# Kernel tuning notes

Hardware: AMD Instinct MI355X
Metric: run time of the kernel (lower is better)

The kernel has to match this reference:

```python
import jax, jax.numpy as jnp
import numpy as np

D_MODEL = 1024
NHEAD = 16
HEAD_DIM = D_MODEL // NHEAD
D_FF = 4096
EPS = 1e-5


def _layernorm(x, g, b):
    mu = jnp.mean(x, axis=-1, keepdims=True)
    var = jnp.mean((x - mu) ** 2, axis=-1, keepdims=True)
    return (x - mu) * jax.lax.rsqrt(var + EPS) * g + b


def setup_inputs() -> dict:
    key = jax.random.key(0)
    ks = jax.random.split(key, 13)
    s = 1.0 / np.sqrt(D_MODEL)
    sf = 1.0 / np.sqrt(D_FF)
    # weights stored as [in, out] (transposed torch Linear)
    return {
        "src": jax.random.normal(ks[0], (4, 2048, D_MODEL), jnp.float32),
        "Wq": jax.random.uniform(ks[1], (D_MODEL, D_MODEL), jnp.float32, -s, s),
        "bq": jnp.zeros((D_MODEL,), jnp.float32),
        "Wk": jax.random.uniform(ks[2], (D_MODEL, D_MODEL), jnp.float32, -s, s),
        "bk": jnp.zeros((D_MODEL,), jnp.float32),
        "Wv": jax.random.uniform(ks[3], (D_MODEL, D_MODEL), jnp.float32, -s, s),
        "bv": jnp.zeros((D_MODEL,), jnp.float32),
        "Wo": jax.random.uniform(ks[4], (D_MODEL, D_MODEL), jnp.float32, -s, s),
        "bo": jnp.zeros((D_MODEL,), jnp.float32),
        "W1": jax.random.uniform(ks[5], (D_MODEL, D_FF), jnp.float32, -s, s),
        "b1": jnp.zeros((D_FF,), jnp.float32),
        "W2": jax.random.uniform(ks[6], (D_FF, D_MODEL), jnp.float32, -sf, sf),
        "b2": jnp.zeros((D_MODEL,), jnp.float32),
        "g1": jnp.ones((D_MODEL,), jnp.float32),
        "be1": jnp.zeros((D_MODEL,), jnp.float32),
        "g2": jnp.ones((D_MODEL,), jnp.float32),
        "be2": jnp.zeros((D_MODEL,), jnp.float32),
    }


def reference(src, Wq, bq, Wk, bk, Wv, bv, Wo, bo, W1, b1, W2, b2, g1, be1, g2, be2):
    B, S, _ = src.shape
    scale = 1.0 / np.sqrt(HEAD_DIM)
    # project and split heads: [B, H, S, Dh]
    def heads(W, b):
        return (src @ W + b).reshape(B, S, NHEAD, HEAD_DIM).transpose(0, 2, 1, 3)
    Q, K, V = heads(Wq, bq), heads(Wk, bk), heads(Wv, bv)
    scores = jnp.einsum('bhqd,bhkd->bhqk', Q, K) * scale
    attn = jax.nn.softmax(scores, axis=-1)
    ctx = jnp.einsum('bhqk,bhkd->bhqd', attn, V)
    ctx = ctx.transpose(0, 2, 1, 3).reshape(B, S, D_MODEL)
    attn_out = ctx @ Wo + bo
    x = _layernorm(src + attn_out, g1, be1)
    ff = jax.nn.relu(x @ W1 + b1) @ W2 + b2
    return _layernorm(x + ff, g2, be2)
```

## Files before the change

### kernel.cpp

```cpp
#include <hip/hip_runtime.h>

typedef __attribute__((ext_vector_type(8))) short bf16x8;
typedef __attribute__((ext_vector_type(4))) float f32x4;
typedef unsigned short u16;
typedef unsigned int u32;

__device__ __forceinline__ u16 f2b(float f) {
  u32 u = __float_as_uint(f);
  u = (u + 0x7fffu + ((u >> 16) & 1u)) >> 16;
  return (u16)u;
}
__device__ __forceinline__ float b2f(u16 b) {
  return __uint_as_float(((u32)b) << 16);
}
__device__ __forceinline__ u32 cvtpk_bf16(float lo, float hi) {
  u32 r;
  asm("v_cvt_pk_bf16_f32 %0, %1, %2" : "=v"(r) : "v"(lo), "v"(hi));
  return r;
}
__device__ __forceinline__ void gload_lds16(const u16* g, u16* l) {
  __builtin_amdgcn_global_load_lds(
      (const __attribute__((address_space(1))) void*)g,
      (__attribute__((address_space(3))) void*)l, 16, 0, 0);
}

__global__ __launch_bounds__(256) void cvt_bf16(const float* __restrict__ in,
                                                u16* __restrict__ out, int n4) {
  int i = blockIdx.x * 256 + threadIdx.x;
  if (i >= n4) return;
  float4 v = ((const float4*)in)[i];
  ushort4 o;
  o.x = f2b(v.x); o.y = f2b(v.y); o.z = f2b(v.z); o.w = f2b(v.w);
  ((ushort4*)out)[i] = o;
}

__global__ __launch_bounds__(256) void transpose_w(const float* __restrict__ in,
                                                   u16* __restrict__ out,
                                                   int R, int C) {
  __shared__ float t[32][33];
  int tid = threadIdx.x, tx = tid & 31, ty = tid >> 5;
  int rb = blockIdx.y * 32, cb = blockIdx.x * 32;
  for (int i = 0; i < 4; i++)
    t[ty + i * 8][tx] = in[(size_t)(rb + ty + i * 8) * C + cb + tx];
  __syncthreads();
  for (int i = 0; i < 4; i++)
    out[(size_t)(cb + ty + i * 8) * R + rb + tx] = f2b(t[tx][ty + i * 8]);
}

__global__ __launch_bounds__(256) void concat3(const float* __restrict__ a,
                                               const float* __restrict__ b,
                                               const float* __restrict__ c,
                                               float* __restrict__ o) {
  int i = blockIdx.x * 256 + threadIdx.x;
  if (i >= 3072) return;
  o[i] = i < 1024 ? a[i] : (i < 2048 ? b[i - 1024] : c[i - 2048]);
}

__device__ __forceinline__ void stage_quarter(const u16* __restrict__ src,
                                              size_t rowbase, int K, int kcol,
                                              u16* dst, int c, int srow, int sg,
                                              int wid) {
  int row_ = c * 64 + srow;
  int gs_ = sg ^ (row_ & 7);
  gload_lds16(src + (rowbase + row_) * K + kcol + gs_ * 8,
              &dst[(c * 64 + wid * 8) * 64]);
}

template <bool PF>
__device__ __forceinline__ void tile_step(
    const u16* sAc, const u16* sBc, u16* sAn, u16* sBn,
    const u16* __restrict__ A, const u16* __restrict__ Bt, size_t abase,
    size_t bbase, int K, int Tn, int wm, int wn, int l16, int lq, int srow,
    int sg, int wid, f32x4 (&acc)[8][4]) {
  __syncthreads();
#pragma unroll
  for (int ks = 0; ks < 2; ++ks) {
    bf16x8 Bf[4], Af[4];
#pragma unroll
    for (int j = 0; j < 4; ++j) {
      int r = wn * 64 + j * 16 + l16;
      Bf[j] = *(const bf16x8*)&sBc[r * 64 + (((ks * 4 + lq) ^ (r & 7)) << 3)];
    }
#pragma unroll
    for (int i = 0; i < 4; ++i) {
      int r = wm * 128 + i * 16 + l16;
      Af[i] = *(const bf16x8*)&sAc[r * 64 + (((ks * 4 + lq) ^ (r & 7)) << 3)];
    }
    if (PF) {
      const u16* src = (ks == 0) ? A : Bt;
      size_t rb = (ks == 0) ? abase : bbase;
      u16* dst = (ks == 0) ? sAn : sBn;
      stage_quarter(src, rb, K, Tn * 64, dst, 0, srow, sg, wid);
      stage_quarter(src, rb, K, Tn * 64, dst, 1, srow, sg, wid);
    }
    __builtin_amdgcn_s_setprio(1);
#pragma unroll
    for (int i = 0; i < 4; ++i)
#pragma unroll
      for (int j = 0; j < 4; ++j)
        acc[i][j] = __builtin_amdgcn_mfma_f32_16x16x32_bf16(Af[i], Bf[j],
                                                            acc[i][j], 0, 0, 0);
    __builtin_amdgcn_s_setprio(0);
#pragma unroll
    for (int i = 0; i < 4; ++i) {
      int r = wm * 128 + 64 + i * 16 + l16;
      Af[i] = *(const bf16x8*)&sAc[r * 64 + (((ks * 4 + lq) ^ (r & 7)) << 3)];
    }
    if (PF) {
      const u16* src = (ks == 0) ? A : Bt;
      size_t rb = (ks == 0) ? abase : bbase;
      u16* dst = (ks == 0) ? sAn : sBn;
      stage_quarter(src, rb, K, Tn * 64, dst, 2, srow, sg, wid);
      stage_quarter(src, rb, K, Tn * 64, dst, 3, srow, sg, wid);
    }
    __builtin_amdgcn_s_setprio(1);
#pragma unroll
    for (int i = 0; i < 4; ++i)
#pragma unroll
      for (int j = 0; j < 4; ++j)
        acc[4 + i][j] = __builtin_amdgcn_mfma_f32_16x16x32_bf16(
            Af[i], Bf[j], acc[4 + i][j], 0, 0, 0);
    __builtin_amdgcn_s_setprio(0);
  }
}

template <int MODE>
__global__ __launch_bounds__(512, 1) void gemm256(const u16* __restrict__ A,
                                                  const u16* __restrict__ Bt,
                                                  const float* __restrict__ bias,
                                                  void* __restrict__ out,
                                                  int M, int N, int K,
                                                  float oscale) {
  __shared__ u16 sA0[256 * 64];
  __shared__ u16 sB0[256 * 64];
  __shared__ u16 sA1[256 * 64];
  __shared__ u16 sB1[256 * 64];
  const int tid = threadIdx.x, lane = tid & 63, wid = tid >> 6;
  const int l16 = lane & 15, lq = lane >> 4;
  const int wm = wid >> 2, wn = wid & 3;
  const size_t abase = (size_t)blockIdx.x * 256;
  const size_t bbase = (size_t)blockIdx.y * 256;
  const int srow = tid >> 3;
  const int sg = tid & 7;
  const int nt = K >> 6;

  f32x4 acc[8][4];
#pragma unroll
  for (int i = 0; i < 8; ++i)
#pragma unroll
    for (int j = 0; j < 4; ++j) acc[i][j] = (f32x4){0.f, 0.f, 0.f, 0.f};

#pragma unroll
  for (int c = 0; c < 4; ++c) {
    stage_quarter(A, abase, K, 0, sA0, c, srow, sg, wid);
    stage_quarter(Bt, bbase, K, 0, sB0, c, srow, sg, wid);
  }

  int T = 0;
  for (; T + 2 < nt; T += 2) {
    tile_step<true>(sA0, sB0, sA1, sB1, A, Bt, abase, bbase, K, T + 1, wm, wn,
                    l16, lq, srow, sg, wid, acc);
    tile_step<true>(sA1, sB1, sA0, sB0, A, Bt, abase, bbase, K, T + 2, wm, wn,
                    l16, lq, srow, sg, wid, acc);
  }
  tile_step<true>(sA0, sB0, sA1, sB1, A, Bt, abase, bbase, K, nt - 1, wm, wn,
                  l16, lq, srow, sg, wid, acc);
  tile_step<false>(sA1, sB1, sA0, sB0, A, Bt, abase, bbase, K, 0, wm, wn, l16,
                   lq, srow, sg, wid, acc);

  const int gmb = blockIdx.x * 256 + wm * 128;
  const int gnb = blockIdx.y * 256 + wn * 64;
#pragma unroll
  for (int i = 0; i < 8; ++i) {
    int gm0 = gmb + i * 16 + lq * 4;
#pragma unroll
    for (int j = 0; j < 4; ++j) {
      int gn = gnb + j * 16 + l16;
      float bv = bias[gn];
#pragma unroll
      for (int r = 0; r < 4; ++r) {
        float v = acc[i][j][r] + bv;
        ((u16*)out)[(size_t)(gm0 + r) * N + gn] = f2b(v > 0.f ? v : 0.f);
      }
    }
  }
}

template <bool PF>
__device__ __forceinline__ void tile_stepR(
    const u16* sAc, const u16* sBc, u16* sAn, u16* sBn,
    const u16* __restrict__ A, const u16* __restrict__ Bt, size_t abase,
    size_t bbase, int K, int Tn, int wm, int wn, int l16, int lq, int srow,
    int sg, int wid, f32x4 (&acc)[4][4]) {
  __syncthreads();
#pragma unroll
  for (int ks = 0; ks < 2; ++ks) {
    bf16x8 Bf[4], Af[4];
#pragma unroll
    for (int j = 0; j < 4; ++j) {
      int r = wn * 64 + j * 16 + l16;
      Bf[j] = *(const bf16x8*)&sBc[r * 64 + (((ks * 4 + lq) ^ (r & 7)) << 3)];
    }
#pragma unroll
    for (int i = 0; i < 4; ++i) {
      int r = wm * 64 + i * 16 + l16;
      Af[i] = *(const bf16x8*)&sAc[r * 64 + (((ks * 4 + lq) ^ (r & 7)) << 3)];
    }
    if (PF) {
      if (ks == 0) {
        stage_quarter(A, abase, K, Tn * 64, sAn, 0, srow, sg, wid);
        stage_quarter(A, abase, K, Tn * 64, sAn, 1, srow, sg, wid);
        stage_quarter(Bt, bbase, K, Tn * 64, sBn, 0, srow, sg, wid);
      } else {
        stage_quarter(Bt, bbase, K, Tn * 64, sBn, 1, srow, sg, wid);
        stage_quarter(Bt, bbase, K, Tn * 64, sBn, 2, srow, sg, wid);
        stage_quarter(Bt, bbase, K, Tn * 64, sBn, 3, srow, sg, wid);
      }
    }
    __builtin_amdgcn_s_setprio(1);
#pragma unroll
    for (int i = 0; i < 4; ++i)
#pragma unroll
      for (int j = 0; j < 4; ++j)
        acc[i][j] = __builtin_amdgcn_mfma_f32_16x16x32_bf16(Af[i], Bf[j],
                                                            acc[i][j], 0, 0, 0);
    __builtin_amdgcn_s_setprio(0);
  }
}

template <int MODE>
__global__ __launch_bounds__(512, 1) void gemmR(const u16* __restrict__ A,
                                                const u16* __restrict__ Bt,
                                                const float* __restrict__ bias,
                                                void* __restrict__ out,
                                                int M, int N, int K,
                                                float oscale) {
  __shared__ u16 sA0[128 * 64];
  __shared__ u16 sB0[256 * 64];
  __shared__ u16 sA1[128 * 64];
  __shared__ u16 sB1[256 * 64];
  const int tid = threadIdx.x, lane = tid & 63, wid = tid >> 6;
  const int l16 = lane & 15, lq = lane >> 4;
  const int wm = wid >> 2, wn = wid & 3;
  const size_t abase = (size_t)blockIdx.x * 128;
  const size_t bbase = (size_t)blockIdx.y * 256;
  const int srow = tid >> 3;
  const int sg = tid & 7;
  const int nt = K >> 6;

  f32x4 acc[4][4];
#pragma unroll
  for (int i = 0; i < 4; ++i)
#pragma unroll
    for (int j = 0; j < 4; ++j) acc[i][j] = (f32x4){0.f, 0.f, 0.f, 0.f};

#pragma unroll
  for (int c = 0; c < 2; ++c) stage_quarter(A, abase, K, 0, sA0, c, srow, sg, wid);
#pragma unroll
  for (int c = 0; c < 4; ++c) stage_quarter(Bt, bbase, K, 0, sB0, c, srow, sg, wid);

  int T = 0;
  for (; T + 2 < nt; T += 2) {
    tile_stepR<true>(sA0, sB0, sA1, sB1, A, Bt, abase, bbase, K, T + 1, wm, wn,
                     l16, lq, srow, sg, wid, acc);
    tile_stepR<true>(sA1, sB1, sA0, sB0, A, Bt, abase, bbase, K, T + 2, wm, wn,
                     l16, lq, srow, sg, wid, acc);
  }
  tile_stepR<true>(sA0, sB0, sA1, sB1, A, Bt, abase, bbase, K, nt - 1, wm, wn,
                   l16, lq, srow, sg, wid, acc);
  tile_stepR<false>(sA1, sB1, sA0, sB0, A, Bt, abase, bbase, K, 0, wm, wn, l16,
                    lq, srow, sg, wid, acc);

  const int gmb = blockIdx.x * 128 + wm * 64;
  const int gnb = blockIdx.y * 256 + wn * 64;
#pragma unroll
  for (int i = 0; i < 4; ++i) {
    int gm0 = gmb + i * 16 + lq * 4;
#pragma unroll
    for (int j = 0; j < 4; ++j) {
      int gn = gnb + j * 16 + l16;
      float bv = bias[gn];
      if constexpr (MODE == 1) {
#pragma unroll
        for (int r = 0; r < 4; ++r)
          ((u16*)out)[(size_t)(gm0 + r) * N + gn] = f2b(acc[i][j][r] + bv);
      } else {
        int sel = gn >> 10;
        int h = (gn & 1023) >> 6, d = gn & 63;
        int b = gm0 >> 11, s = gm0 & 2047;
        u16* o = (u16*)out + (size_t)sel * (8u << 20);
        if (sel == 2) {
          ushort4 w;
          w.x = f2b(acc[i][j][0] + bv);
          w.y = f2b(acc[i][j][1] + bv);
          w.z = f2b(acc[i][j][2] + bv);
          w.w = f2b(acc[i][j][3] + bv);
          *(ushort4*)(o + ((size_t)((b * 16 + h) * 64 + d)) * 2048 + s) = w;
        } else {
          float sc = (sel == 0) ? oscale : 1.f;
#pragma unroll
          for (int r = 0; r < 4; ++r)
            o[((size_t)(b * 16 + h) * 2048 + s + r) * 64 + d] =
                f2b((acc[i][j][r] + bv) * sc);
        }
      }
    }
  }
}

__global__ __launch_bounds__(256) void attn_fwd(const u16* __restrict__ Q,
                                                const u16* __restrict__ Kb,
                                                const u16* __restrict__ Vt,
                                                u16* __restrict__ ctx) {
  __shared__ u16 sK[64][64];
  __shared__ u16 sV[64][64];
  __shared__ u16 sP[4][16][72];
  const int tid = threadIdx.x, lane = tid & 63, wid = tid >> 6;
  const int l16 = lane & 15, lq = lane >> 4;
  const int bh = blockIdx.y, qt = blockIdx.x;
  const size_t base = (size_t)bh * (2048 * 64);
  const int xk = l16 & 7;

  bf16x8 qf[2];
  {
    int qrow = qt * 64 + wid * 16 + l16;
    qf[0] = *(const bf16x8*)(Q + base + (size_t)qrow * 64 + lq * 8);
    qf[1] = *(const bf16x8*)(Q + base + (size_t)qrow * 64 + 32 + lq * 8);
  }
  f32x4 o[4];
#pragma unroll
  for (int j = 0; j < 4; j++) o[j] = (f32x4){0.f, 0.f, 0.f, 0.f};
  float mrow = -3e38f, lrow = 0.f;

  const int srow_c = lane >> 3;
  const int sslot = ((lane & 7) ^ srow_c) * 8;

  for (int kv0 = 0; kv0 < 2048; kv0 += 64) {
    __syncthreads();
#pragma unroll
    for (int c = 0; c < 2; c++) {
      int row = wid * 16 + c * 8 + srow_c;
      gload_lds16(Kb + base + (size_t)(kv0 + row) * 64 + sslot, &sK[wid * 16 + c * 8][0]);
      gload_lds16(Vt + base + (size_t)row * 2048 + kv0 + sslot, &sV[wid * 16 + c * 8][0]);
    }
    __syncthreads();

    f32x4 sf[4];
#pragma unroll
    for (int j = 0; j < 4; j++) sf[j] = (f32x4){0.f, 0.f, 0.f, 0.f};
#pragma unroll
    for (int ks = 0; ks < 2; ks++)
#pragma unroll
      for (int j = 0; j < 4; j++) {
        bf16x8 kf = *(const bf16x8*)&sK[j * 16 + l16][((ks * 4 + lq) ^ xk) * 8];
        sf[j] = __builtin_amdgcn_mfma_f32_16x16x32_bf16(kf, qf[ks], sf[j], 0, 0, 0);
      }

    float pm = fmaxf(fmaxf(fmaxf(sf[0][0], sf[0][1]), fmaxf(sf[0][2], sf[0][3])),
                     fmaxf(fmaxf(sf[1][0], sf[1][1]), fmaxf(sf[1][2], sf[1][3])));
    pm = fmaxf(pm,
               fmaxf(fmaxf(fmaxf(sf[2][0], sf[2][1]), fmaxf(sf[2][2], sf[2][3])),
                     fmaxf(fmaxf(sf[3][0], sf[3][1]), fmaxf(sf[3][2], sf[3][3]))));
    pm = fmaxf(pm, __shfl_xor(pm, 16));
    pm = fmaxf(pm, __shfl_xor(pm, 32));

    if (!__all(pm - mrow <= 8.f)) {
      float mn = fmaxf(mrow, pm);
      float osc = __builtin_amdgcn_exp2f(mrow - mn);
      mrow = mn;
      lrow *= osc;
      float oscr[4];
#pragma unroll
      for (int r = 0; r < 4; r++) oscr[r] = __shfl(osc, lq * 4 + r);
#pragma unroll
      for (int j = 0; j < 4; j++)
#pragma unroll
        for (int r = 0; r < 4; r++) o[j][r] *= oscr[r];
    }

    float rs = 0.f;
#pragma unroll
    for (int j = 0; j < 4; j++) {
      float p0 = __builtin_amdgcn_exp2f(sf[j][0] - mrow);
      float p1 = __builtin_amdgcn_exp2f(sf[j][1] - mrow);
      float p2 = __builtin_amdgcn_exp2f(sf[j][2] - mrow);
      float p3 = __builtin_amdgcn_exp2f(sf[j][3] - mrow);
      rs += (p0 + p1) + (p2 + p3);
      uint2 w;
      w.x = cvtpk_bf16(p0, p1);
      w.y = cvtpk_bf16(p2, p3);
      *(uint2*)&sP[wid][l16][j * 16 + lq * 4] = w;
    }
    rs += __shfl_xor(rs, 16);
    rs += __shfl_xor(rs, 32);
    lrow += rs;

#pragma unroll
    for (int ks = 0; ks < 2; ks++) {
      bf16x8 pf = *(const bf16x8*)&sP[wid][l16][ks * 32 + lq * 8];
#pragma unroll
      for (int j = 0; j < 4; j++) {
        bf16x8 vf = *(const bf16x8*)&sV[j * 16 + l16][((ks * 4 + lq) ^ xk) * 8];
        o[j] = __builtin_amdgcn_mfma_f32_16x16x32_bf16(pf, vf, o[j], 0, 0, 0);
      }
    }
  }

  float lval[4];
#pragma unroll
  for (int r = 0; r < 4; r++) lval[r] = 1.f / __shfl(lrow, lq * 4 + r);
  const int b = bh >> 4, h = bh & 15;
#pragma unroll
  for (int j = 0; j < 4; j++)
#pragma unroll
    for (int r = 0; r < 4; r++) {
      int srow = qt * 64 + wid * 16 + lq * 4 + r;
      int d = j * 16 + l16;
      ctx[((size_t)(b * 2048 + srow)) * 1024 + h * 64 + d] = f2b(o[j][r] * lval[r]);
    }
}

template <int A_BF16, int B_BF16, int WRITE_F32>
__global__ __launch_bounds__(256) void ln_res(const void* __restrict__ a,
                                              const void* __restrict__ bsrc,
                                              const float* __restrict__ g,
                                              const float* __restrict__ be,
                                              float* __restrict__ outf,
                                              u16* __restrict__ outb) {
  const int row = blockIdx.x, tid = threadIdx.x;
  const size_t off = (size_t)row * 1024 + tid * 4;
  float4 x;
  if constexpr (A_BF16) {
    ushort4 av = *(const ushort4*)((const u16*)a + off);
    x.x = b2f(av.x); x.y = b2f(av.y); x.z = b2f(av.z); x.w = b2f(av.w);
  } else {
    x = *(const float4*)((const float*)a + off);
  }
  if constexpr (B_BF16) {
    ushort4 bv = *(const ushort4*)((const u16*)bsrc + off);
    x.x += b2f(bv.x); x.y += b2f(bv.y); x.z += b2f(bv.z); x.w += b2f(bv.w);
  } else {
    float4 bb = *(const float4*)((const float*)bsrc + off);
    x.x += bb.x; x.y += bb.y; x.z += bb.z; x.w += bb.w;
  }
  float s = x.x + x.y + x.z + x.w;
  float s2 = x.x * x.x + x.y * x.y + x.z * x.z + x.w * x.w;
  for (int o = 1; o < 64; o <<= 1) {
    s += __shfl_xor(s, o);
    s2 += __shfl_xor(s2, o);
  }
  __shared__ float rbuf[8];
  int lane = tid & 63, wid = tid >> 6;
  if (lane == 0) { rbuf[wid] = s; rbuf[4 + wid] = s2; }
  __syncthreads();
  s = rbuf[0] + rbuf[1] + rbuf[2] + rbuf[3];
  s2 = rbuf[4] + rbuf[5] + rbuf[6] + rbuf[7];
  float mu = s * (1.f / 1024.f);
  float var = s2 * (1.f / 1024.f) - mu * mu;
  float rstd = rsqrtf(var + 1e-5f);
  int c = tid * 4;
  float y0 = (x.x - mu) * rstd * g[c + 0] + be[c + 0];
  float y1 = (x.y - mu) * rstd * g[c + 1] + be[c + 1];
  float y2 = (x.z - mu) * rstd * g[c + 2] + be[c + 2];
  float y3 = (x.w - mu) * rstd * g[c + 3] + be[c + 3];
  if constexpr (WRITE_F32) {
    float4 y; y.x = y0; y.y = y1; y.z = y2; y.w = y3;
    *(float4*)(outf + off) = y;
  } else {
    ushort4 yb;
    yb.x = f2b(y0); yb.y = f2b(y1); yb.z = f2b(y2); yb.w = f2b(y3);
    *(ushort4*)(outb + off) = yb;
  }
}

extern "C" void kernel_launch(void* const* d_in, const int* in_sizes, int n_in,
                              void* d_out, int out_size, void* d_ws, size_t ws_size,
                              hipStream_t stream) {
  const float* src = (const float*)d_in[0];
  const float* Wq = (const float*)d_in[1];
  const float* bq = (const float*)d_in[2];
  const float* Wk = (const float*)d_in[3];
  const float* bk = (const float*)d_in[4];
  const float* Wv = (const float*)d_in[5];
  const float* bv = (const float*)d_in[6];
  const float* Wo = (const float*)d_in[7];
  const float* bo = (const float*)d_in[8];
  const float* W1 = (const float*)d_in[9];
  const float* b1 = (const float*)d_in[10];
  const float* W2 = (const float*)d_in[11];
  const float* b2 = (const float*)d_in[12];
  const float* g1 = (const float*)d_in[13];
  const float* be1 = (const float*)d_in[14];
  const float* g2 = (const float*)d_in[15];
  const float* be2 = (const float*)d_in[16];
  float* out = (float*)d_out;
  char* ws = (char*)d_ws;
  const size_t MB = 1ull << 20;

  u16* XB    = (u16*)(ws + 0);
  u16* WQKVT = (u16*)(ws + 16 * MB);
  u16* WOT   = (u16*)(ws + 22 * MB);
  u16* W1T   = (u16*)(ws + 24 * MB);
  u16* W2T   = (u16*)(ws + 32 * MB);
  float* bqkv = (float*)(ws + 40 * MB);
  u16* Qb    = (u16*)(ws + 41 * MB);
  u16* Kbuf  = (u16*)(ws + 57 * MB);
  u16* Vt    = (u16*)(ws + 73 * MB);
  u16* CTX   = XB;
  u16* AO    = (u16*)(ws + 41 * MB);
  u16* H1    = (u16*)(ws + 57 * MB);
  u16* XBUF  = (u16*)(ws + 121 * MB);
  u16* FF    = XB;

  const float QSCALE = 0.125f * 1.44269504088896340736f;

  cvt_bf16<<<dim3(8192), dim3(256), 0, stream>>>(src, XB, 2097152);
  transpose_w<<<dim3(32, 32), dim3(256), 0, stream>>>(Wq, WQKVT, 1024, 1024);
  transpose_w<<<dim3(32, 32), dim3(256), 0, stream>>>(Wk, WQKVT + 1024 * 1024, 1024, 1024);
  transpose_w<<<dim3(32, 32), dim3(256), 0, stream>>>(Wv, WQKVT + 2048 * 1024, 1024, 1024);
  transpose_w<<<dim3(32, 32), dim3(256), 0, stream>>>(Wo, WOT, 1024, 1024);
  transpose_w<<<dim3(128, 32), dim3(256), 0, stream>>>(W1, W1T, 1024, 4096);
  transpose_w<<<dim3(32, 128), dim3(256), 0, stream>>>(W2, W2T, 4096, 1024);
  concat3<<<dim3(12), dim3(256), 0, stream>>>(bq, bk, bv, bqkv);

  gemmR<6><<<dim3(64, 12), dim3(512), 0, stream>>>(XB, WQKVT, bqkv, Qb,
                                                   8192, 3072, 1024, QSCALE);
  attn_fwd<<<dim3(32, 64), dim3(256), 0, stream>>>(Qb, Kbuf, Vt, CTX);
  gemmR<1><<<dim3(64, 4), dim3(512), 0, stream>>>(CTX, WOT, bo, AO,
                                                  8192, 1024, 1024, 1.0f);
  ln_res<0, 1, 0><<<dim3(8192), dim3(256), 0, stream>>>(src, AO, g1, be1, nullptr, XBUF);
  gemm256<2><<<dim3(32, 16), dim3(512), 0, stream>>>(XBUF, W1T, b1, H1,
                                                     8192, 4096, 1024, 1.0f);
  gemmR<1><<<dim3(64, 4), dim3(512), 0, stream>>>(H1, W2T, b2, FF,
                                                  8192, 1024, 4096, 1.0f);
  ln_res<1, 1, 1><<<dim3(8192), dim3(256), 0, stream>>>(XBUF, FF, g2, be2, out, nullptr);
}
```

Baseline: 388.7 us.

## Swizzle GEMM blocks across XCDs and register-prefetch K/V tiles in attention

```diff
diff --git a/kernel.cpp b/kernel.cpp
--- a/kernel.cpp
+++ b/kernel.cpp
@@ -66,6 +66,10 @@
               &dst[(c * 64 + wid * 8) * 64]);
 }
 
+__device__ __forceinline__ int xcd_swz(int flat, int nwg) {
+  return (flat & 7) * (nwg >> 3) + (flat >> 3);
+}
+
 template <bool PF>
 __device__ __forceinline__ void tile_step(
     const u16* sAc, const u16* sBc, u16* sAn, u16* sBn,
@@ -130,16 +134,18 @@
                                                   const float* __restrict__ bias,
                                                   void* __restrict__ out,
                                                   int M, int N, int K,
-                                                  float oscale) {
+                                                  int nby, float oscale) {
   __shared__ u16 sA0[256 * 64];
   __shared__ u16 sB0[256 * 64];
   __shared__ u16 sA1[256 * 64];
   __shared__ u16 sB1[256 * 64];
+  const int swz = xcd_swz(blockIdx.x, gridDim.x);
+  const int bx = swz / nby, by = swz % nby;
   const int tid = threadIdx.x, lane = tid & 63, wid = tid >> 6;
   const int l16 = lane & 15, lq = lane >> 4;
   const int wm = wid >> 2, wn = wid & 3;
-  const size_t abase = (size_t)blockIdx.x * 256;
-  const size_t bbase = (size_t)blockIdx.y * 256;
+  const size_t abase = (size_t)bx * 256;
+  const size_t bbase = (size_t)by * 256;
   const int srow = tid >> 3;
   const int sg = tid & 7;
   const int nt = K >> 6;
@@ -168,8 +174,8 @@
   tile_step<false>(sA1, sB1, sA0, sB0, A, Bt, abase, bbase, K, 0, wm, wn, l16,
                    lq, srow, sg, wid, acc);
 
-  const int gmb = blockIdx.x * 256 + wm * 128;
-  const int gnb = blockIdx.y * 256 + wn * 64;
+  const int gmb = bx * 256 + wm * 128;
+  const int gnb = by * 256 + wn * 64;
 #pragma unroll
   for (int i = 0; i < 8; ++i) {
     int gm0 = gmb + i * 16 + lq * 4;
@@ -234,16 +240,18 @@
                                                 const float* __restrict__ bias,
                                                 void* __restrict__ out,
                                                 int M, int N, int K,
-                                                float oscale) {
+                                                int nby, float oscale) {
   __shared__ u16 sA0[128 * 64];
   __shared__ u16 sB0[256 * 64];
   __shared__ u16 sA1[128 * 64];
   __shared__ u16 sB1[256 * 64];
+  const int swz = xcd_swz(blockIdx.x, gridDim.x);
+  const int bx = swz / nby, by = swz % nby;
   const int tid = threadIdx.x, lane = tid & 63, wid = tid >> 6;
   const int l16 = lane & 15, lq = lane >> 4;
   const int wm = wid >> 2, wn = wid & 3;
-  const size_t abase = (size_t)blockIdx.x * 128;
-  const size_t bbase = (size_t)blockIdx.y * 256;
+  const size_t abase = (size_t)bx * 128;
+  const size_t bbase = (size_t)by * 256;
   const int srow = tid >> 3;
   const int sg = tid & 7;
   const int nt = K >> 6;
@@ -271,8 +279,8 @@
   tile_stepR<false>(sA1, sB1, sA0, sB0, A, Bt, abase, bbase, K, 0, wm, wn, l16,
                     lq, srow, sg, wid, acc);
 
-  const int gmb = blockIdx.x * 128 + wm * 64;
-  const int gnb = blockIdx.y * 256 + wn * 64;
+  const int gmb = bx * 128 + wm * 64;
+  const int gnb = by * 256 + wn * 64;
 #pragma unroll
   for (int i = 0; i < 4; ++i) {
     int gm0 = gmb + i * 16 + lq * 4;
@@ -333,21 +341,39 @@
   float mrow = -3e38f, lrow = 0.f;
 
   const int srow_c = lane >> 3;
-  const int sslot = ((lane & 7) ^ srow_c) * 8;
+  const int sg8 = ((lane & 7) ^ srow_c) * 8;
+  const int row0 = wid * 16 + srow_c, row1 = row0 + 8;
+  const int wslot = (lane & 7) * 8;
+
+  const u16* kp0 = Kb + base + (size_t)row0 * 64 + sg8;
+  const u16* kp1 = Kb + base + (size_t)row1 * 64 + sg8;
+  const u16* vp0 = Vt + base + (size_t)row0 * 2048 + sg8;
+  const u16* vp1 = Vt + base + (size_t)row1 * 2048 + sg8;
+
+  uint4 rk0 = *(const uint4*)kp0;
+  uint4 rk1 = *(const uint4*)kp1;
+  uint4 rv0 = *(const uint4*)vp0;
+  uint4 rv1 = *(const uint4*)vp1;
 
   for (int kv0 = 0; kv0 < 2048; kv0 += 64) {
     __syncthreads();
-#pragma unroll
-    for (int c = 0; c < 2; c++) {
-      int row = wid * 16 + c * 8 + srow_c;
-      gload_lds16(Kb + base + (size_t)(kv0 + row) * 64 + sslot, &sK[wid * 16 + c * 8][0]);
-      gload_lds16(Vt + base + (size_t)row * 2048 + kv0 + sslot, &sV[wid * 16 + c * 8][0]);
+    *(uint4*)&sK[row0][wslot] = rk0;
+    *(uint4*)&sK[row1][wslot] = rk1;
+    *(uint4*)&sV[row0][wslot] = rv0;
+    *(uint4*)&sV[row1][wslot] = rv1;
+    if (kv0 + 64 < 2048) {
+      int kn = kv0 + 64;
+      rk0 = *(const uint4*)(kp0 + (size_t)kn * 64);
+      rk1 = *(const uint4*)(kp1 + (size_t)kn * 64);
+      rv0 = *(const uint4*)(vp0 + kn);
+      rv1 = *(const uint4*)(vp1 + kn);
     }
     __syncthreads();
 
     f32x4 sf[4];
 #pragma unroll
     for (int j = 0; j < 4; j++) sf[j] = (f32x4){0.f, 0.f, 0.f, 0.f};
+    __builtin_amdgcn_s_setprio(1);
 #pragma unroll
     for (int ks = 0; ks < 2; ks++)
 #pragma unroll
@@ -355,6 +381,7 @@
         bf16x8 kf = *(const bf16x8*)&sK[j * 16 + l16][((ks * 4 + lq) ^ xk) * 8];
         sf[j] = __builtin_amdgcn_mfma_f32_16x16x32_bf16(kf, qf[ks], sf[j], 0, 0, 0);
       }
+    __builtin_amdgcn_s_setprio(0);
 
     float pm = fmaxf(fmaxf(fmaxf(sf[0][0], sf[0][1]), fmaxf(sf[0][2], sf[0][3])),
                      fmaxf(fmaxf(sf[1][0], sf[1][1]), fmaxf(sf[1][2], sf[1][3])));
@@ -395,6 +422,7 @@
     rs += __shfl_xor(rs, 32);
     lrow += rs;
 
+    __builtin_amdgcn_s_setprio(1);
 #pragma unroll
     for (int ks = 0; ks < 2; ks++) {
       bf16x8 pf = *(const bf16x8*)&sP[wid][l16][ks * 32 + lq * 8];
@@ -404,6 +432,7 @@
         o[j] = __builtin_amdgcn_mfma_f32_16x16x32_bf16(pf, vf, o[j], 0, 0, 0);
       }
     }
+    __builtin_amdgcn_s_setprio(0);
   }
 
   float lval[4];
@@ -523,15 +552,15 @@
   transpose_w<<<dim3(32, 128), dim3(256), 0, stream>>>(W2, W2T, 4096, 1024);
   concat3<<<dim3(12), dim3(256), 0, stream>>>(bq, bk, bv, bqkv);
 
-  gemmR<6><<<dim3(64, 12), dim3(512), 0, stream>>>(XB, WQKVT, bqkv, Qb,
-                                                   8192, 3072, 1024, QSCALE);
+  gemmR<6><<<dim3(768), dim3(512), 0, stream>>>(XB, WQKVT, bqkv, Qb,
+                                                8192, 3072, 1024, 12, QSCALE);
   attn_fwd<<<dim3(32, 64), dim3(256), 0, stream>>>(Qb, Kbuf, Vt, CTX);
-  gemmR<1><<<dim3(64, 4), dim3(512), 0, stream>>>(CTX, WOT, bo, AO,
-                                                  8192, 1024, 1024, 1.0f);
+  gemmR<1><<<dim3(256), dim3(512), 0, stream>>>(CTX, WOT, bo, AO,
+                                                8192, 1024, 1024, 4, 1.0f);
   ln_res<0, 1, 0><<<dim3(8192), dim3(256), 0, stream>>>(src, AO, g1, be1, nullptr, XBUF);
-  gemm256<2><<<dim3(32, 16), dim3(512), 0, stream>>>(XBUF, W1T, b1, H1,
-                                                     8192, 4096, 1024, 1.0f);
-  gemmR<1><<<dim3(64, 4), dim3(512), 0, stream>>>(H1, W2T, b2, FF,
-                                                  8192, 1024, 4096, 1.0f);
+  gemm256<2><<<dim3(512), dim3(512), 0, stream>>>(XBUF, W1T, b1, H1,
+                                                  8192, 4096, 1024, 16, 1.0f);
+  gemmR<1><<<dim3(256), dim3(512), 0, stream>>>(H1, W2T, b2, FF,
+                                                8192, 1024, 4096, 4, 1.0f);
   ln_res<1, 1, 1><<<dim3(8192), dim3(256), 0, stream>>>(XBUF, FF, g2, be2, out, nullptr);
 }
```

New measurement: 404.2 us. 1.04x slower.
